# Performance work log

Hardware: AMD Instinct MI355X
Metric: run time of the kernel (lower is better)

The kernel has to match this reference:

```python
import jax, jax.numpy as jnp
import numpy as np

E = 20000       # num edges (nodes of the edge-adjacency graph)
FDIM = 128      # edge_feature_dim
D = 16          # stalk_dim ('diagonal' => mlp output dim = D)
P = 300000      # number of adjacent (i, j) pairs extracted from L1
EPS = 1e-5      # LayerNorm eps


def _xavier(key, fan_in, fan_out):
    lim = np.sqrt(6.0 / (fan_in + fan_out)).astype(np.float32)
    return jax.random.uniform(key, (fan_in, fan_out), jnp.float32, -lim, lim)


def _layernorm(x, g, b):
    mu = jnp.mean(x, axis=-1, keepdims=True)
    var = jnp.mean((x - mu) ** 2, axis=-1, keepdims=True)
    return (x - mu) * jax.lax.rsqrt(var + EPS) * g + b


def setup_inputs() -> dict:
    key = jax.random.key(0)
    ks = jax.random.split(key, 8)
    return {
        "edge_features": jax.random.normal(ks[0], (E, FDIM), jnp.float32),
        "pair_i": jax.random.randint(ks[1], (P,), 0, E),
        "pair_j": jax.random.randint(ks[2], (P,), 0, E),
        # MLP: Linear(2F,64) -> LN -> ReLU -> Linear(64,32) -> LN -> ReLU -> Linear(32,D)
        "W1": _xavier(ks[3], 2 * FDIM, 64), "b1": jnp.zeros((64,), jnp.float32),
        "g1": jnp.ones((64,), jnp.float32), "be1": jnp.zeros((64,), jnp.float32),
        "W2": _xavier(ks[4], 64, 32), "b2": jnp.zeros((32,), jnp.float32),
        "g2": jnp.ones((32,), jnp.float32), "be2": jnp.zeros((32,), jnp.float32),
        "W3": _xavier(ks[5], 32, D), "b3": jnp.zeros((D,), jnp.float32),
    }


def reference(edge_features, pair_i, pair_j, W1, b1, g1, be1, W2, b2, g2, be2, W3, b3):
    # Gather the two edge feature vectors per adjacent pair and concat: [P, 2F]
    x = jnp.concatenate([edge_features[pair_i], edge_features[pair_j]], axis=1)
    h = jax.nn.relu(_layernorm(x @ W1 + b1, g1, be1))      # [P, 64]
    h = jax.nn.relu(_layernorm(h @ W2 + b2, g2, be2))      # [P, 32]
    params = h @ W3 + b3                                    # [P, D]
    # diagonal sheaf: F_ij = diag(params) for every pair, batched (diag_embed)
    return params[:, :, None] * jnp.eye(D, dtype=params.dtype)  # [P, D, D]
```

## Files before the change

### kernel.cpp

```cpp
#include <hip/hip_runtime.h>
#include <hip/hip_fp16.h>

typedef float f32x4 __attribute__((ext_vector_type(4)));

__global__ void bad_map_marker(float* out) {
    if (threadIdx.x == 0 && blockIdx.x == 0) out[0] = 1.0e6f;
}

__device__ __forceinline__ void mlp_tail_compute(float* h, float* pr, int D,
        const float* g1, const float* be1,
        const float* W2, const float* b2,
        const float* g2, const float* be2,
        const float* W3, const float* b3) {
    float s = 0.f, ss = 0.f;
    #pragma unroll
    for (int d = 0; d < 64; ++d) { s += h[d]; ss += h[d] * h[d]; }
    float mu  = s * (1.f / 64.f);
    float inv = rsqrtf(ss * (1.f / 64.f) - mu * mu + 1e-5f);
    #pragma unroll
    for (int d = 0; d < 64; ++d)
        h[d] = fmaxf((h[d] - mu) * inv * g1[d] + be1[d], 0.f);

    float a2[32];
    const float4* w2v = (const float4*)W2;
    #pragma unroll
    for (int n = 0; n < 32; ++n) a2[n] = b2[n];
    for (int k = 0; k < 64; ++k) {
        float hk = h[k];
        #pragma unroll
        for (int q = 0; q < 8; ++q) {
            float4 w = w2v[k * 8 + q];
            a2[4 * q + 0] += hk * w.x;
            a2[4 * q + 1] += hk * w.y;
            a2[4 * q + 2] += hk * w.z;
            a2[4 * q + 3] += hk * w.w;
        }
    }
    s = 0.f; ss = 0.f;
    #pragma unroll
    for (int n = 0; n < 32; ++n) { s += a2[n]; ss += a2[n] * a2[n]; }
    mu  = s * (1.f / 32.f);
    inv = rsqrtf(ss * (1.f / 32.f) - mu * mu + 1e-5f);
    #pragma unroll
    for (int n = 0; n < 32; ++n)
        a2[n] = fmaxf((a2[n] - mu) * inv * g2[n] + be2[n], 0.f);

    for (int d = 0; d < D; ++d) pr[d] = b3[d];
    for (int k = 0; k < 32; ++k) {
        float hk = a2[k];
        const float* wr = W3 + k * D;
        for (int d = 0; d < D; ++d) pr[d] += hk * wr[d];
    }
}

__device__ __forceinline__ void store_diag16_f32_256(const float* pp, float* out, int P) {
    const int t = threadIdx.x;
    f32x4* outv = (f32x4*)out + (size_t)blockIdx.x * 16384;
    const int pbase = blockIdx.x * 256;
    #pragma unroll 8
    for (int it = 0; it < 64; ++it) {
        int g = it * 256 + t;
        int pl = g >> 6;
        int rem = g & 63;
        int d = rem >> 2;
        int c4 = rem & 3;
        float val = pp[pl * 17 + d];
        bool on = (d >> 2) == c4;
        f32x4 v;
        v.x = (on && (d & 3) == 0) ? val : 0.f;
        v.y = (on && (d & 3) == 1) ? val : 0.f;
        v.z = (on && (d & 3) == 2) ? val : 0.f;
        v.w = (on && (d & 3) == 3) ? val : 0.f;
        if (pbase + pl < P) __builtin_nontemporal_store(v, &outv[g]);
    }
}

__global__ __launch_bounds__(256)
void precompute_y(const float* __restrict__ ef, const float* __restrict__ W1,
                  const float* __restrict__ b1, __half* __restrict__ Ya,
                  __half* __restrict__ Yb, int E) {
    __shared__ __align__(16) float el[64 * 132];
    const int t = threadIdx.x;
    const int ebase = blockIdx.x * 64;

    for (int idx = t; idx < 2048; idx += 256) {
        int er = idx >> 5, ec = idx & 31;
        if (ebase + er < E)
            *((float4*)(el + er * 132) + ec) =
                *((const float4*)(ef + (size_t)(ebase + er) * 128) + ec);
    }
    __syncthreads();

    const int cg = t & 15;
    const int eg = t >> 4;
    const int half_ = cg >> 3;
    const int col64 = (cg & 7) * 8;

    float acc[4][8];
    #pragma unroll
    for (int i = 0; i < 4; ++i)
        #pragma unroll
        for (int c = 0; c < 8; ++c) acc[i][c] = 0.f;

    const float* wbase = W1 + (size_t)half_ * 128 * 64 + col64;
    #pragma unroll 4
    for (int k = 0; k < 128; ++k) {
        float4 w0 = *(const float4*)(wbase + (size_t)k * 64);
        float4 w1 = *(const float4*)(wbase + (size_t)k * 64 + 4);
        float wv[8] = {w0.x, w0.y, w0.z, w0.w, w1.x, w1.y, w1.z, w1.w};
        #pragma unroll
        for (int i = 0; i < 4; ++i) {
            float a = el[(eg * 4 + i) * 132 + k];
            #pragma unroll
            for (int c = 0; c < 8; ++c) acc[i][c] += a * wv[c];
        }
    }

    float bb[8];
    #pragma unroll
    for (int c = 0; c < 8; ++c) bb[c] = (half_ == 0) ? b1[col64 + c] : 0.f;
    __half* base = (half_ == 0) ? Ya : Yb;
    #pragma unroll
    for (int i = 0; i < 4; ++i) {
        int e = ebase + eg * 4 + i;
        if (e < E) {
            __half* dst = base + (size_t)e * 64 + col64;
            __half2 hv[4];
            #pragma unroll
            for (int c = 0; c < 4; ++c)
                hv[c] = __floats2half2_rn(acc[i][2 * c] + bb[2 * c],
                                          acc[i][2 * c + 1] + bb[2 * c + 1]);
            *(float4*)dst = *(float4*)hv;
        }
    }
}

__global__ __launch_bounds__(256)
void sheaf_pairs(const int* __restrict__ pi, const int* __restrict__ pj,
                 const __half* __restrict__ Ya, const __half* __restrict__ Yb,
                 const float* __restrict__ g1, const float* __restrict__ be1,
                 const float* __restrict__ W2, const float* __restrict__ b2,
                 const float* __restrict__ g2, const float* __restrict__ be2,
                 const float* __restrict__ W3, const float* __restrict__ b3,
                 float* __restrict__ out, int P) {
    __shared__ float pp[256 * 17];
    __shared__ __align__(16) float w2s[64 * 32];
    __shared__ __align__(16) float w3s[32 * 16];
    __shared__ float g1s[64], be1s[64], b2s[32], g2s[32], be2s[32], b3s[16];

    const int t = threadIdx.x;
    int p = blockIdx.x * 256 + t;
    int pc = p < P ? p : P - 1;
    int i = pi[pc], j = pj[pc];

    const float4* y1 = (const float4*)(Ya + (size_t)i * 64);
    const float4* y2 = (const float4*)(Yb + (size_t)j * 64);
    float4 ra[8], rb[8];
    #pragma unroll
    for (int q = 0; q < 8; ++q) { ra[q] = y1[q]; rb[q] = y2[q]; }

    {
        const float4* s2 = (const float4*)W2;
        float4* d2 = (float4*)w2s;
        d2[t]       = s2[t];
        d2[t + 256] = s2[t + 256];
        if (t < 128) ((float4*)w3s)[t] = ((const float4*)W3)[t];
        if (t < 64)                 { g1s[t] = g1[t]; be1s[t] = be1[t]; }
        else if (t < 96)            b2s[t - 64]   = b2[t - 64];
        else if (t < 128)           g2s[t - 96]   = g2[t - 96];
        else if (t < 160)           be2s[t - 128] = be2[t - 128];
        else if (t < 176)           b3s[t - 160]  = b3[t - 160];
    }

    float h[64];
    #pragma unroll
    for (int q = 0; q < 8; ++q) {
        const __half2* ha = (const __half2*)&ra[q];
        const __half2* hb = (const __half2*)&rb[q];
        #pragma unroll
        for (int u = 0; u < 4; ++u) {
            float2 fa = __half22float2(ha[u]);
            float2 fb = __half22float2(hb[u]);
            h[8 * q + 2 * u + 0] = fa.x + fb.x;
            h[8 * q + 2 * u + 1] = fa.y + fb.y;
        }
    }
    __syncthreads();

    float pr[16];
    mlp_tail_compute(h, pr, 16, g1s, be1s, w2s, b2s, g2s, be2s, w3s, b3s);
    #pragma unroll
    for (int d = 0; d < 16; ++d) pp[t * 17 + d] = pr[d];
    __syncthreads();
    store_diag16_f32_256(pp, out, P);
}

__global__ __launch_bounds__(256)
void sheaf_generic(const float* __restrict__ ef,
                   const int* __restrict__ pi, const int* __restrict__ pj,
                   const float* __restrict__ W1, const float* __restrict__ b1,
                   const float* __restrict__ g1, const float* __restrict__ be1,
                   const float* __restrict__ W2, const float* __restrict__ b2,
                   const float* __restrict__ g2, const float* __restrict__ be2,
                   const float* __restrict__ W3, const float* __restrict__ b3,
                   float* __restrict__ out, int P, int F, int D) {
    __shared__ float pp[256 * 17];
    int p = blockIdx.x * 256 + threadIdx.x;
    int pc = p < P ? p : P - 1;
    int i = pi[pc], j = pj[pc];
    const float* efi = ef + (size_t)i * F;
    const float* efj = ef + (size_t)j * F;
    float h[64];
    #pragma unroll
    for (int n = 0; n < 64; ++n) h[n] = b1[n];
    for (int k = 0; k < F; ++k) {
        float ei = efi[k];
        float ej = efj[k];
        const float* wi = W1 + (size_t)k * 64;
        const float* wj = W1 + (size_t)(F + k) * 64;
        #pragma unroll
        for (int n = 0; n < 64; ++n) h[n] += ei * wi[n] + ej * wj[n];
    }
    float pr[32];
    mlp_tail_compute(h, pr, D, g1, be1, W2, b2, g2, be2, W3, b3);

    if (D == 16) {
        #pragma unroll
        for (int d = 0; d < 16; ++d) pp[threadIdx.x * 17 + d] = pr[d];
        __syncthreads();
        store_diag16_f32_256(pp, out, P);
    } else {
        if (p < P) {
            float* po = out + (size_t)p * D * D;
            for (int r = 0; r < D; ++r) {
                float dv = pr[r];
                for (int c = 0; c < D; ++c) po[r * D + c] = (r == c) ? dv : 0.f;
            }
        }
    }
}

struct Map { int ef, pi, pj, w1, b1, g1, be1, w2, b2, g2, be2, w3, b3; };

static bool validate_map(const Map& m, const int* s, int n_in, long out_size,
                         int* Fo, int* Eo, int* Do, int* Po) {
    if (n_in < 13) return false;
    if (s[m.b1] != 64 || s[m.g1] != 64 || s[m.be1] != 64) return false;
    if (s[m.b2] != 32 || s[m.g2] != 32 || s[m.be2] != 32) return false;
    if (s[m.w2] != 64 * 32) return false;
    long w1 = s[m.w1];
    if (w1 <= 0 || (w1 % 128) != 0) return false;
    long F = w1 / 128;
    if (F <= 0) return false;
    int D = s[m.b3];
    if (D <= 0 || D > 32) return false;
    if (s[m.w3] != 32 * D) return false;
    long P = s[m.pi];
    if (P <= 0 || s[m.pj] != P) return false;
    long ef = s[m.ef];
    if (ef <= 0 || (ef % F) != 0) return false;
    long E = ef / F;
    if (out_size != P * D * D) return false;
    *Fo = (int)F; *Eo = (int)E; *Do = D; *Po = (int)P;
    return true;
}

extern "C" void kernel_launch(void* const* d_in, const int* in_sizes, int n_in,
                              void* d_out, int out_size, void* d_ws, size_t ws_size,
                              hipStream_t stream) {
    const Map pos   = {0, 1, 2, 3, 4, 5, 6, 7, 8, 9, 10, 11, 12};
    const Map alpha = {8, 11, 12, 0, 3, 9, 6, 1, 4, 10, 7, 2, 5};

    int F = 0, E = 0, D = 0, P = 0;
    Map m;
    if (validate_map(pos, in_sizes, n_in, (long)out_size, &F, &E, &D, &P)) {
        m = pos;
    } else if (validate_map(alpha, in_sizes, n_in, (long)out_size, &F, &E, &D, &P)) {
        m = alpha;
    } else {
        bad_map_marker<<<dim3(1), dim3(64), 0, stream>>>((float*)d_out);
        return;
    }

    const float* ef  = (const float*)d_in[m.ef];
    const int*   pi  = (const int*)d_in[m.pi];
    const int*   pj  = (const int*)d_in[m.pj];
    const float* W1  = (const float*)d_in[m.w1];
    const float* b1  = (const float*)d_in[m.b1];
    const float* g1  = (const float*)d_in[m.g1];
    const float* be1 = (const float*)d_in[m.be1];
    const float* W2  = (const float*)d_in[m.w2];
    const float* b2  = (const float*)d_in[m.b2];
    const float* g2  = (const float*)d_in[m.g2];
    const float* be2 = (const float*)d_in[m.be2];
    const float* W3  = (const float*)d_in[m.w3];
    const float* b3  = (const float*)d_in[m.b3];
    float* out = (float*)d_out;

    const size_t ya_bytes = (size_t)E * 64 * sizeof(__half);
    const size_t y_bytes  = 2 * ya_bytes;

    if (F == 128 && D == 16 && ws_size >= y_bytes) {
        __half* Ya = (__half*)d_ws;
        __half* Yb = (__half*)((char*)d_ws + ya_bytes);
        precompute_y<<<dim3((E + 63) / 64), dim3(256), 0, stream>>>(ef, W1, b1, Ya, Yb, E);
        sheaf_pairs<<<dim3((P + 255) / 256), dim3(256), 0, stream>>>(
            pi, pj, Ya, Yb, g1, be1, W2, b2, g2, be2, W3, b3, out, P);
    } else {
        sheaf_generic<<<dim3((P + 255) / 256), dim3(256), 0, stream>>>(
            ef, pi, pj, W1, b1, g1, be1, W2, b2, g2, be2, W3, b3, out, P, F, D);
    }
}
```

Baseline: 378.8 us.

## Sort pairs by first index via counting sort before the MLP kernel

Adds a counting sort of pairs by pair_i (histogram, single-block scan, atomic scatter) and a sorted variant of the pair kernel that gathers rows in sorted order and scatters outputs to their original positions. The aim is better cache locality on the Ya gathers. The cost is four extra launches, atomics, and a serial one-block scan. Output stores become scattered 1KB rows instead of contiguous ones. The output is 300000x256 floats (about 307MB), so the kernel is likely bound by output writes, and the gather gain from sorting is probably small.

New measurement: 464.9 us. +22.7%, slower.

```diff
diff --git a/kernel.cpp b/kernel.cpp
--- a/kernel.cpp
+++ b/kernel.cpp
@@ -132,6 +132,141 @@
                                           acc[i][2 * c + 1] + bb[2 * c + 1]);
             *(float4*)dst = *(float4*)hv;
         }
+    }
+}
+
+__global__ __launch_bounds__(256)
+void zero_hist(int* __restrict__ hist, int E) {
+    int idx = blockIdx.x * 256 + threadIdx.x;
+    if (idx < E) hist[idx] = 0;
+}
+
+__global__ __launch_bounds__(256)
+void hist_pairs(const int* __restrict__ pi, int* __restrict__ hist, int P) {
+    int p = blockIdx.x * 256 + threadIdx.x;
+    if (p < P) atomicAdd(&hist[pi[p]], 1);
+}
+
+__global__ __launch_bounds__(1024)
+void scan_hist(const int* __restrict__ hist, int* __restrict__ offs, int E) {
+    __shared__ int lds[1024];
+    const int tid = threadIdx.x;
+    const int chunk = (E + 1023) >> 10;
+    const int base = tid * chunk;
+    int sum = 0;
+    for (int m = 0; m < chunk; ++m) {
+        int idx = base + m;
+        if (idx < E) sum += hist[idx];
+    }
+    lds[tid] = sum;
+    __syncthreads();
+    for (int off = 1; off < 1024; off <<= 1) {
+        int v = (tid >= off) ? lds[tid - off] : 0;
+        __syncthreads();
+        lds[tid] += v;
+        __syncthreads();
+    }
+    int run = lds[tid] - sum;
+    for (int m = 0; m < chunk; ++m) {
+        int idx = base + m;
+        if (idx < E) {
+            offs[idx] = run;
+            run += hist[idx];
+        }
+    }
+}
+
+__global__ __launch_bounds__(256)
+void scatter_pairs(const int* __restrict__ pi, const int* __restrict__ pj,
+                   int* __restrict__ offs, int* __restrict__ si,
+                   int* __restrict__ sj, int* __restrict__ dst, int P) {
+    int p = blockIdx.x * 256 + threadIdx.x;
+    if (p < P) {
+        int bin = pi[p];
+        int pos = atomicAdd(&offs[bin], 1);
+        si[pos]  = bin;
+        sj[pos]  = pj[p];
+        dst[pos] = p;
+    }
+}
+
+__global__ __launch_bounds__(256)
+void sheaf_pairs_sorted(const int* __restrict__ si, const int* __restrict__ sj,
+                        const int* __restrict__ dst,
+                        const __half* __restrict__ Ya, const __half* __restrict__ Yb,
+                        const float* __restrict__ g1, const float* __restrict__ be1,
+                        const float* __restrict__ W2, const float* __restrict__ b2,
+                        const float* __restrict__ g2, const float* __restrict__ be2,
+                        const float* __restrict__ W3, const float* __restrict__ b3,
+                        float* __restrict__ out, int P) {
+    __shared__ float pp[256 * 17];
+    __shared__ int dstS[256];
+    __shared__ __align__(16) float w2s[64 * 32];
+    __shared__ __align__(16) float w3s[32 * 16];
+    __shared__ float g1s[64], be1s[64], b2s[32], g2s[32], be2s[32], b3s[16];
+
+    const int t = threadIdx.x;
+    int pos = blockIdx.x * 256 + t;
+    int pc  = pos < P ? pos : P - 1;
+    int i = si[pc], j = sj[pc];
+    dstS[t] = dst[pc];
+
+    const float4* y1 = (const float4*)(Ya + (size_t)i * 64);
+    const float4* y2 = (const float4*)(Yb + (size_t)j * 64);
+    float4 ra[8], rb[8];
+    #pragma unroll
+    for (int q = 0; q < 8; ++q) { ra[q] = y1[q]; rb[q] = y2[q]; }
+
+    {
+        const float4* s2 = (const float4*)W2;
+        float4* d2 = (float4*)w2s;
+        d2[t]       = s2[t];
+        d2[t + 256] = s2[t + 256];
+        if (t < 128) ((float4*)w3s)[t] = ((const float4*)W3)[t];
+        if (t < 64)                 { g1s[t] = g1[t]; be1s[t] = be1[t]; }
+        else if (t < 96)            b2s[t - 64]   = b2[t - 64];
+        else if (t < 128)           g2s[t - 96]   = g2[t - 96];
+        else if (t < 160)           be2s[t - 128] = be2[t - 128];
+        else if (t < 176)           b3s[t - 160]  = b3[t - 160];
+    }
+
+    float h[64];
+    #pragma unroll
+    for (int q = 0; q < 8; ++q) {
+        const __half2* ha = (const __half2*)&ra[q];
+        const __half2* hb = (const __half2*)&rb[q];
+        #pragma unroll
+        for (int u = 0; u < 4; ++u) {
+            float2 fa = __half22float2(ha[u]);
+            float2 fb = __half22float2(hb[u]);
+            h[8 * q + 2 * u + 0] = fa.x + fb.x;
+            h[8 * q + 2 * u + 1] = fa.y + fb.y;
+        }
+    }
+    __syncthreads();
+
+    float pr[16];
+    mlp_tail_compute(h, pr, 16, g1s, be1s, w2s, b2s, g2s, be2s, w3s, b3s);
+    #pragma unroll
+    for (int d = 0; d < 16; ++d) pp[t * 17 + d] = pr[d];
+    __syncthreads();
+
+    const int wave = t >> 6;
+    const int lane = t & 63;
+    const int d  = lane >> 2;
+    const int c4 = lane & 3;
+    f32x4* out4 = (f32x4*)out;
+    #pragma unroll 8
+    for (int g = 0; g < 64; ++g) {
+        int lp = g * 4 + wave;
+        float val = pp[lp * 17 + d];
+        bool on = (d >> 2) == c4;
+        f32x4 v;
+        v.x = (on && (d & 3) == 0) ? val : 0.f;
+        v.y = (on && (d & 3) == 1) ? val : 0.f;
+        v.z = (on && (d & 3) == 2) ? val : 0.f;
+        v.w = (on && (d & 3) == 3) ? val : 0.f;
+        __builtin_nontemporal_store(v, &out4[(size_t)dstS[lp] * 64 + lane]);
     }
 }
 
@@ -265,6 +400,8 @@
     return true;
 }
 
+static inline size_t al256(size_t x) { return (x + 255) & ~(size_t)255; }
+
 extern "C" void kernel_launch(void* const* d_in, const int* in_sizes, int n_in,
                               void* d_out, int out_size, void* d_ws, size_t ws_size,
                               hipStream_t stream) {
@@ -297,15 +434,38 @@
     const float* b3  = (const float*)d_in[m.b3];
     float* out = (float*)d_out;
 
-    const size_t ya_bytes = (size_t)E * 64 * sizeof(__half);
-    const size_t y_bytes  = 2 * ya_bytes;
-
-    if (F == 128 && D == 16 && ws_size >= y_bytes) {
-        __half* Ya = (__half*)d_ws;
-        __half* Yb = (__half*)((char*)d_ws + ya_bytes);
+    const size_t o_ya   = 0;
+    const size_t o_yb   = o_ya  + al256((size_t)E * 64 * 2);
+    const size_t o_hist = o_yb  + al256((size_t)E * 64 * 2);
+    const size_t o_offs = o_hist + al256((size_t)E * 4);
+    const size_t o_si   = o_offs + al256((size_t)E * 4);
+    const size_t o_sj   = o_si  + al256((size_t)P * 4);
+    const size_t o_dst  = o_sj  + al256((size_t)P * 4);
+    const size_t need_sorted = o_dst + al256((size_t)P * 4);
+    const size_t need_plain  = o_hist;
+
+    if (F == 128 && D == 16 && ws_size >= need_plain) {
+        __half* Ya = (__half*)((char*)d_ws + o_ya);
+        __half* Yb = (__half*)((char*)d_ws + o_yb);
         precompute_y<<<dim3((E + 63) / 64), dim3(256), 0, stream>>>(ef, W1, b1, Ya, Yb, E);
-        sheaf_pairs<<<dim3((P + 255) / 256), dim3(256), 0, stream>>>(
-            pi, pj, Ya, Yb, g1, be1, W2, b2, g2, be2, W3, b3, out, P);
+
+        const int pblk = (P + 255) / 256;
+        if (ws_size >= need_sorted) {
+            int* hist = (int*)((char*)d_ws + o_hist);
+            int* offs = (int*)((char*)d_ws + o_offs);
+            int* si   = (int*)((char*)d_ws + o_si);
+            int* sj   = (int*)((char*)d_ws + o_sj);
+            int* dst  = (int*)((char*)d_ws + o_dst);
+            zero_hist<<<dim3((E + 255) / 256), dim3(256), 0, stream>>>(hist, E);
+            hist_pairs<<<dim3(pblk), dim3(256), 0, stream>>>(pi, hist, P);
+            scan_hist<<<dim3(1), dim3(1024), 0, stream>>>(hist, offs, E);
+            scatter_pairs<<<dim3(pblk), dim3(256), 0, stream>>>(pi, pj, offs, si, sj, dst, P);
+            sheaf_pairs_sorted<<<dim3(pblk), dim3(256), 0, stream>>>(
+                si, sj, dst, Ya, Yb, g1, be1, W2, b2, g2, be2, W3, b3, out, P);
+        } else {
+            sheaf_pairs<<<dim3(pblk), dim3(256), 0, stream>>>(
+                pi, pj, Ya, Yb, g1, be1, W2, b2, g2, be2, W3, b3, out, P);
+        }
     } else {
         sheaf_generic<<<dim3((P + 255) / 256), dim3(256), 0, stream>>>(
             ef, pi, pj, W1, b1, g1, be1, W2, b2, g2, be2, W3, b3, out, P, F, D);
```
